# Kernel tuning notes

Hardware: AMD Instinct MI355X
Metric: run time of the kernel (lower is better)

## Reference

```python
import jax, jax.numpy as jnp
import numpy as np

N_NODES = 10000
N_EDGES = 128000


def _edge_conv(x, row, col, edge_attr, w1, b1, w2, b2):
    # gather endpoints, concat edge features, 2-layer MLP per edge
    m = jnp.concatenate([x[row], x[col], edge_attr], axis=1)  # [E, 2*in+edge]
    m = jax.nn.relu(m @ w1 + b1) @ w2 + b2                    # [E, out]
    # scatter-mean onto source nodes (flow='target_to_source' -> aggregate on row)
    n = x.shape[0]
    s = jax.ops.segment_sum(m, row, num_segments=n)
    cnt = jax.ops.segment_sum(jnp.ones((row.shape[0], 1), m.dtype), row, num_segments=n)
    out = s / jnp.maximum(cnt, 1.0)
    return out, m


def setup_inputs() -> dict:
    key = jax.random.key(0)
    ks = jax.random.split(key, 24)
    f = jnp.float32

    def lin(kw, kb, fan_in, fan_out):
        lim = 1.0 / np.sqrt(fan_in)
        w = jax.random.uniform(kw, (fan_in, fan_out), f, -lim, lim)
        b = jax.random.uniform(kb, (fan_out,), f, -lim, lim)
        return w, b

    inp = {}
    inp['x_org'] = jax.random.normal(ks[0], (N_NODES, 256), f)
    inp['x_rot'] = jax.random.normal(ks[1], (N_NODES, 4), f)
    inp['edge_index'] = jax.random.randint(ks[2], (2, N_EDGES), 0, N_NODES, jnp.int64 if jax.config.jax_enable_x64 else jnp.int32)
    inp['edge_attr'] = jax.random.normal(ks[3], (N_EDGES, 640), f)
    inp['edge_rot'] = jax.random.normal(ks[4], (N_EDGES, 4), f)

    # conv1: Linear(2*260+644=1164, 64), Linear(64, 64)
    inp['c1_w1'], inp['c1_b1'] = lin(ks[5], ks[6], 1164, 64)
    inp['c1_w2'], inp['c1_b2'] = lin(ks[7], ks[8], 64, 64)
    # conv2: Linear(2*64+704=832, 64), Linear(64, 64)
    inp['c2_w1'], inp['c2_b1'] = lin(ks[9], ks[10], 832, 64)
    inp['c2_w2'], inp['c2_b2'] = lin(ks[11], ks[12], 64, 64)
    # conv3: Linear(2*128+128=384, 64), Linear(64, 64)
    inp['c3_w1'], inp['c3_b1'] = lin(ks[13], ks[14], 384, 64)
    inp['c3_w2'], inp['c3_b2'] = lin(ks[15], ks[16], 64, 64)
    # conv4: Linear(384, 64), Linear(64, 64)
    inp['c4_w1'], inp['c4_b1'] = lin(ks[17], ks[18], 384, 64)
    inp['c4_w2'], inp['c4_b2'] = lin(ks[19], ks[20], 64, 64)
    # lin1: Linear(64, 4)
    inp['lin1_w'], inp['lin1_b'] = lin(ks[21], ks[22], 64, 4)
    # edge_fc: Linear(64, 32) -> ReLU -> Linear(32, 1)
    k23 = jax.random.split(ks[23], 4)
    inp['efc_w1'], inp['efc_b1'] = lin(k23[0], k23[1], 64, 32)
    inp['efc_w2'], inp['efc_b2'] = lin(k23[2], k23[3], 32, 1)
    return inp


def reference(x_org, x_rot, edge_index, edge_attr, edge_rot,
              c1_w1, c1_b1, c1_w2, c1_b2,
              c2_w1, c2_b1, c2_w2, c2_b2,
              c3_w1, c3_b1, c3_w2, c3_b2,
              c4_w1, c4_b1, c4_w2, c4_b2,
              lin1_w, lin1_b, efc_w1, efc_b1, efc_w2, efc_b2):
    node_feat = jnp.concatenate([x_org, x_rot], axis=1)
    edge_feat = jnp.concatenate([edge_attr, edge_rot], axis=1)
    row, col = edge_index[0], edge_index[1]
    E = edge_index.shape[1]

    x1, edge_x1 = _edge_conv(node_feat, row, col, edge_feat, c1_w1, c1_b1, c1_w2, c1_b2)
    edge_x1 = jax.nn.relu(edge_x1)

    x2, edge_x2 = _edge_conv(x1, row, col, jnp.concatenate([edge_attr, edge_x1], axis=1),
                             c2_w1, c2_b1, c2_w2, c2_b2)
    x2 = jax.nn.relu(x2)
    edge_x2 = jax.nn.relu(edge_x2)

    x3, edge_x3 = _edge_conv(jnp.concatenate([x2, x1], axis=1), row, col,
                             jnp.concatenate([edge_x2, edge_x1], axis=1),
                             c3_w1, c3_b1, c3_w2, c3_b2)
    x3 = jax.nn.relu(x3)
    edge_x3 = jax.nn.relu(edge_x3)

    x4, edge_x4 = _edge_conv(jnp.concatenate([x3, x2], axis=1), row, col,
                             jnp.concatenate([edge_x3, edge_x2], axis=1),
                             c4_w1, c4_b1, c4_w2, c4_b2)
    x4 = jax.nn.relu(x4)

    x = x4 @ lin1_w + lin1_b  # [N, 4]
    h = edge_x4[: E // 2] + edge_x4[E // 2:]
    pred_edge_res = jax.nn.relu(h @ efc_w1 + efc_b1) @ efc_w2 + efc_b2  # [E/2, 1]

    # F.normalize(x, p=2, dim=1)
    x = x / jnp.maximum(jnp.linalg.norm(x, axis=1, keepdims=True), 1e-12)
    return x, pred_edge_res
```

## Files before the change

### kernel.cpp

```cpp
#include <hip/hip_runtime.h>
#include <stdint.h>


#define N_NODES 10000
#define N_EDGES 128000
#define E_HALF  64000
#define NBLK    1000

typedef unsigned short u16;

using bf16x8 = __attribute__((ext_vector_type(8))) short;
using f32x4  = __attribute__((ext_vector_type(4))) float;

#define MFMA16(A, B, C) C = __builtin_amdgcn_mfma_f32_16x16x32_bf16(A, B, C, 0, 0, 0)

__device__ __align__(256) float g_acc[N_NODES * 64];
__device__ __align__(256) float g_deg[N_NODES];
__device__ __align__(256) float g_P[N_NODES * 128];
__device__ __align__(256) float g_x1[N_NODES * 64];
__device__ __align__(256) float g_x2[N_NODES * 64];
__device__ __align__(256) float g_x3[N_NODES * 64];
__device__ __align__(256) u16  g_fragA[(size_t)NBLK * 16384];
__device__ __align__(256) u16  g_fragB[(size_t)NBLK * 16384];
__device__ __align__(256) float g_Q2 [(size_t)N_EDGES * 64];
__device__ __align__(256) float g_ex4[(size_t)N_EDGES * 64];
__device__ __align__(256) u16  g_wpA_hi[2 * 4096];
__device__ __align__(256) u16  g_wpA_lo[2 * 4096];
__device__ __align__(256) u16  g_wp2_hi[4096];
__device__ __align__(256) u16  g_wp2_lo[4096];
__device__ __align__(256) u16  g_wnp_hi[4 * 8192];
__device__ __align__(256) u16  g_wnp_lo[4 * 8192];
__device__ __align__(256) u16  g_wpC_hi[10 * 8192];
__device__ __align__(256) u16  g_wpC_lo[10 * 8192];
__device__ __align__(256) int g_row[N_EDGES];
__device__ __align__(256) int g_col[N_EDGES];
__device__ int g_mode;
__device__ int g_is64;

__device__ __forceinline__ float b2f(u16 u) {
    return __uint_as_float(((unsigned int)u) << 16);
}
__device__ __forceinline__ u16 f2b(float f) {
    unsigned int u = __float_as_uint(f);
    u += 0x7FFFu + ((u >> 16) & 1u);
    return (u16)(u >> 16);
}
__device__ __forceinline__ float ldf(const u16* p)   { return b2f(*p); }
__device__ __forceinline__ float ldf(const float* p) { return *p; }
__device__ __forceinline__ void  stf(u16* p, float v)   { *p = f2b(v); }
__device__ __forceinline__ void  stf(float* p, float v) { *p = v; }

__device__ __forceinline__ float4 load4(const float* p) { return *(const float4*)p; }
__device__ __forceinline__ float4 load4(const u16* p) {
    ushort4 v = *(const ushort4*)p;
    return make_float4(b2f(v.x), b2f(v.y), b2f(v.z), b2f(v.w));
}

template<int KTB>
__device__ __forceinline__ int swz(int b) {
    return b ^ ((b >> 4) & 3) ^ (((b >> KTB) & 1) << 2);
}

__device__ __forceinline__ void split_pack(float4 v, uint2& hi, uint2& lo) {
    unsigned int ux = __float_as_uint(v.x), uy = __float_as_uint(v.y);
    unsigned int uz = __float_as_uint(v.z), uw = __float_as_uint(v.w);
    unsigned int hx = ux & 0xFFFF0000u, hy = uy & 0xFFFF0000u;
    unsigned int hz = uz & 0xFFFF0000u, hw = uw & 0xFFFF0000u;
    hi.x = (hx >> 16) | hy;
    hi.y = (hz >> 16) | hw;
    u16 lx = f2b(v.x - __uint_as_float(hx));
    u16 ly = f2b(v.y - __uint_as_float(hy));
    u16 lz = f2b(v.z - __uint_as_float(hz));
    u16 lw = f2b(v.w - __uint_as_float(hw));
    lo.x = (unsigned int)lx | ((unsigned int)ly << 16);
    lo.y = (unsigned int)lz | ((unsigned int)lw << 16);
}

__global__ void detect_kernel(const void* x_org_v, const int* __restrict__ eidx) {
    const u16* w = (const u16*)x_org_v;
    const int t = threadIdx.x;
    int ok = 0;
    for (int i = t; i < 128; i += 64) {
        u16 v = w[i];
        int ex = (v >> 7) & 0xFF;
        ok += ((ex >= 0x68 && ex <= 0x88) || ((v & 0x7FFFu) == 0)) ? 1 : 0;
    }
    #pragma unroll
    for (int off = 32; off >= 1; off >>= 1) ok += __shfl_xor(ok, off);
    bool allz = true;
    for (int i = t; i < 2048; i += 64) allz = allz && (eidx[2 * i + 1] == 0);
    unsigned long long m = __ballot(allz);
    if (t == 0) {
        g_mode = (ok >= 110) ? 0 : 1;
        g_is64 = (m == ~0ull) ? 1 : 0;
    }
}

__global__ void cvt_idx(const int* __restrict__ eidx) {
    const int e = blockIdx.x * 256 + threadIdx.x;
    if (g_is64) {
        g_row[e] = eidx[2 * e];
        g_col[e] = eidx[2 * (e + N_EDGES)];
    } else {
        g_row[e] = eidx[e];
        g_col[e] = eidx[e + N_EDGES];
    }
}

__global__ void zero_all() {
    const int i = blockIdx.x * 256 + threadIdx.x;
    g_acc[i] = 0.f;
    if (i < N_NODES) g_deg[i] = 0.f;
}

__global__ void deg_kernel() {
    const int e = blockIdx.x * 256 + threadIdx.x;
    if (e < N_EDGES) atomicAdd(&g_deg[g_row[e]], 1.0f);
}

template<typename TW>
__device__ void pack_w_body(const TW* w1a, const TW* w2, const TW* w1b,
                            int we, int ns, int hioff, int nsn, int nsc) {
    const int idx = blockIdx.x * 256 + threadIdx.x;
    const int t1 = ns * 4096;
    const int t2 = t1 + 4096;
    const int t3 = t2 + nsn * 8192;
    if (idx < t1) {
        const int s = idx >> 12;
        const int rem = idx & 4095;
        const int kt = rem >> 11, ct = (rem >> 9) & 3, l = (rem >> 3) & 63, r = rem & 7;
        const int k = s * 64 + kt * 32 + 4 * (l >> 4) + (r & 3) + 16 * (r >> 2);
        const float v = ldf(w1a + (size_t)(we + k) * 64 + ct * 16 + (l & 15));
        const u16 hh = f2b(v);
        g_wpA_hi[idx] = hh;
        g_wpA_lo[idx] = f2b(v - b2f(hh));
    } else if (idx < t2) {
        const int rem = idx - t1;
        const int kt = rem >> 11, ct = (rem >> 9) & 3, l = (rem >> 3) & 63, r = rem & 7;
        const int k = kt * 32 + 4 * (l >> 4) + (r & 3) + 16 * (r >> 2);
        const float v = ldf(w2 + (size_t)k * 64 + ct * 16 + (l & 15));
        const u16 hh = f2b(v);
        g_wp2_hi[rem] = hh;
        g_wp2_lo[rem] = f2b(v - b2f(hh));
    } else if (idx < t3) {
        const int rem = idx - t2;
        const int s = rem >> 13;
        const int kt = (rem >> 12) & 1, ct = (rem >> 9) & 7, l = (rem >> 3) & 63, r = rem & 7;
        const int k = s * 64 + kt * 32 + 4 * (l >> 4) + (r & 3) + 16 * (r >> 2);
        const int col = ct * 16 + (l & 15);
        const int row = (col < 64) ? k : (hioff + k);
        const float v = ldf(w1a + (size_t)row * 64 + (col & 63));
        const u16 hh = f2b(v);
        g_wnp_hi[rem] = hh;
        g_wnp_lo[rem] = f2b(v - b2f(hh));
    } else if (idx < t3 + nsc * 8192) {
        const int rem = idx - t3;
        const int s = rem >> 13;
        const int kt = (rem >> 12) & 1, ct = (rem >> 9) & 7, l = (rem >> 3) & 63, r = rem & 7;
        const int k = s * 64 + kt * 32 + 4 * (l >> 4) + (r & 3) + 16 * (r >> 2);
        const int col = ct * 16 + (l & 15);
        float v;
        if (col < 64) v = ldf(w1a + (size_t)(520 + k) * 64 + col);
        else          v = ldf(w1b + (size_t)(128 + k) * 64 + (col - 64));
        const u16 hh = f2b(v);
        g_wpC_hi[rem] = hh;
        g_wpC_lo[rem] = f2b(v - b2f(hh));
    }
}
__global__ void pack_w_k(const void* w1a, const void* w2, const void* w1b,
                         int we, int ns, int hioff, int nsn, int nsc) {
    if (g_mode == 0)
        pack_w_body<u16>((const u16*)w1a, (const u16*)w2, (const u16*)w1b,
                         we, ns, hioff, nsn, nsc);
    else
        pack_w_body<float>((const float*)w1a, (const float*)w2, (const float*)w1b,
                         we, ns, hioff, nsn, nsc);
}

template<typename TA, int NS1, int NS2, bool TAIL>
__device__ void node_mfma_body(u16* smA, float* smrot, float* smwt,
        const TA* A1, const float* A2, const TA* rotsrc, const TA* w1, float* P) {
    constexpr int NS = NS1 + NS2;
    const int t = threadIdx.x;
    const int lane = t & 63, wid = t >> 6;
    const int q = lane >> 4, n = lane & 15;
    const int r0b = blockIdx.x * 64;

    if constexpr (TAIL) {
        if (t < 64) {
            const int rr = min(r0b + t, N_NODES - 1);
            float4 v = load4(rotsrc + (size_t)rr * 4);
            smrot[t * 4 + 0] = v.x; smrot[t * 4 + 1] = v.y;
            smrot[t * 4 + 2] = v.z; smrot[t * 4 + 3] = v.w;
        }
        for (int i = t; i < 512; i += 256) {
            const int j = i >> 7, c = i & 127;
            const int row = (c < 64) ? (256 + j) : (516 + j);
            smwt[i] = ldf(w1 + (size_t)row * 64 + (c & 63));
        }
    }

    f32x4 acc[8];
    #pragma unroll
    for (int ct = 0; ct < 8; ++ct) acc[ct] = (f32x4){0.f, 0.f, 0.f, 0.f};

    const int eb = t >> 4;
    const int cc = t & 15;

    for (int s = 0; s < NS; ++s) {
        #pragma unroll
        for (int p = 0; p < 4; ++p) {
            const int e = p * 16 + eb;
            const int row = min(r0b + e, N_NODES - 1);
            float4 v;
            if constexpr (NS2 > 0)
                v = (s < NS1) ? load4(A1 + (size_t)row * (NS1 * 64) + s * 64 + cc * 4)
                              : load4(A2 + (size_t)row * (NS2 * 64) + (s - NS1) * 64 + cc * 4);
            else
                v = load4(A1 + (size_t)row * (NS1 * 64) + s * 64 + cc * 4);
            uint2 hi, lo; split_pack(v, hi, lo);
            const int blk = ((cc >> 3) * 4 + (e >> 4)) * 64 + (cc & 3) * 16 + (e & 15);
            const int elem = swz<8>(blk) * 8 + ((cc >> 2) & 1) * 4;
            *(uint2*)&smA[elem]        = hi;
            *(uint2*)&smA[elem + 4096] = lo;
        }
        __syncthreads();
        const u16* wph = g_wnp_hi + s * 8192;
        const u16* wpl = g_wnp_lo + s * 8192;
        #pragma unroll
        for (int kt = 0; kt < 2; ++kt) {
            const int ad = swz<8>((kt * 4 + wid) * 64 + lane) * 8;
            bf16x8 ah = *(const bf16x8*)&smA[ad];
            bf16x8 al = *(const bf16x8*)&smA[ad + 4096];
            #pragma unroll
            for (int ct = 0; ct < 8; ++ct) {
                bf16x8 bh = *(const bf16x8*)&wph[(kt * 8 + ct) * 512 + lane * 8];
                bf16x8 bl = *(const bf16x8*)&wpl[(kt * 8 + ct) * 512 + lane * 8];
                MFMA16(ah, bh, acc[ct]);
                MFMA16(al, bh, acc[ct]);
                MFMA16(ah, bl, acc[ct]);
            }
        }
        __syncthreads();
    }

    #pragma unroll
    for (int ct = 0; ct < 8; ++ct) {
        #pragma unroll
        for (int i = 0; i < 4; ++i) {
            const int rl = wid * 16 + 4 * q + i;
            const int row = r0b + rl;
            const int col = ct * 16 + n;
            float v = acc[ct][i];
            if constexpr (TAIL)
                v += smrot[rl * 4 + 0] * smwt[0 * 128 + col]
                   + smrot[rl * 4 + 1] * smwt[1 * 128 + col]
                   + smrot[rl * 4 + 2] * smwt[2 * 128 + col]
                   + smrot[rl * 4 + 3] * smwt[3 * 128 + col];
            if (row < N_NODES) P[(size_t)row * 128 + col] = v;
        }
    }
}

template<int NS1, bool TAIL>
__global__ void __launch_bounds__(256) node_mfma_in(
        const void* A1, const void* rotsrc, const void* w1, float* __restrict__ P) {
    __shared__ u16 smA[8192];
    __shared__ float smrot[256], smwt[512];
    if (g_mode == 0)
        node_mfma_body<u16, NS1, 0, TAIL>(smA, smrot, smwt, (const u16*)A1,
            nullptr, (const u16*)rotsrc, (const u16*)w1, P);
    else
        node_mfma_body<float, NS1, 0, TAIL>(smA, smrot, smwt, (const float*)A1,
            nullptr, (const float*)rotsrc, (const float*)w1, P);
}

template<int NS1, int NS2>
__global__ void __launch_bounds__(256) node_mfma_ws(
        const float* A1, const float* A2, float* __restrict__ P) {
    __shared__ u16 smA[8192];
    __shared__ float smrot[256], smwt[512];
    node_mfma_body<float, NS1, NS2, false>(smA, smrot, smwt, A1, A2,
        (const float*)nullptr, (const float*)nullptr, P);
}

__device__ __forceinline__ void frag_store_o(u16* smA, int wid, int lane,
        const f32x4 (&oacc)[2][4], u16* Fdst, int blkid) {
    const int q = lane >> 4, n = lane & 15;
    #pragma unroll
    for (int rt = 0; rt < 2; ++rt)
        #pragma unroll
        for (int ct = 0; ct < 4; ++ct)
            #pragma unroll
            for (int i = 0; i < 4; ++i) {
                float v = fmaxf(oacc[rt][ct][i], 0.f);
                unsigned int hb = __float_as_uint(v) & 0xFFFF0000u;
                const u16 hh = (u16)(hb >> 16);
                const u16 hl = f2b(v - __uint_as_float(hb));
                const int off = wid * 4096
                              + (((ct >> 1) * 2 + rt) * 64 + (n >> 2) * 16 + 4 * q + i) * 8
                              + (ct & 1) * 4 + (n & 3);
                smA[off]        = hh;
                smA[off + 2048] = hl;
            }
    #pragma unroll
    for (int kt = 0; kt < 2; ++kt)
        #pragma unroll
        for (int rtl = 0; rtl < 2; ++rtl) {
            const int src = wid * 4096 + ((kt * 2 + rtl) * 64 + lane) * 8;
            bf16x8 h8 = *(const bf16x8*)&smA[src];
            bf16x8 l8 = *(const bf16x8*)&smA[src + 2048];
            const size_t gb = (size_t)blkid * 16384
                            + (size_t)(kt * 8 + wid * 2 + rtl) * 512 + lane * 8;
            *(bf16x8*)&Fdst[gb]        = h8;
            *(bf16x8*)&Fdst[gb + 8192] = l8;
        }
}

template<typename TA, typename TW>
__device__ void edge_c1_body(u16* smA, int* srow, int* scol,
        float* b1s, float* b2s, float* rot, float* wtl,
        const TA* efa, const TA* rotsrc,
        const TW* w1, const TW* b1v, const TW* b2v) {
    const int t = threadIdx.x;
    const int lane = t & 63, wid = t >> 6;
    const int q = lane >> 4, n = lane & 15;
    const int e0 = blockIdx.x * 128;

    if (t < 128) srow[t] = g_row[e0 + t];
    else         scol[t - 128] = g_col[e0 + t - 128];
    if (t >= 128 && t < 192) b1s[t - 128] = ldf(b1v + (t - 128));
    if (t >= 192)            b2s[t - 192] = ldf(b2v + (t - 192));
    if (t < 128) {
        float4 r4 = load4(rotsrc + (size_t)(e0 + t) * 4);
        rot[t * 4 + 0] = r4.x; rot[t * 4 + 1] = r4.y;
        rot[t * 4 + 2] = r4.z; rot[t * 4 + 3] = r4.w;
    }
    wtl[t] = ldf(w1 + (size_t)(1160 + (t >> 6)) * 64 + (t & 63));

    f32x4 acc[2][8];
    #pragma unroll
    for (int a_ = 0; a_ < 2; ++a_)
        #pragma unroll
        for (int b_ = 0; b_ < 8; ++b_)
            acc[a_][b_] = (f32x4){0.f, 0.f, 0.f, 0.f};

    const int eb = t >> 4;
    const int cc = t & 15;

    for (int s = 0; s < 10; ++s) {
        #pragma unroll
        for (int p = 0; p < 8; ++p) {
            const int e = p * 16 + eb;
            float4 v = load4(efa + (size_t)(e0 + e) * 640 + s * 64 + cc * 4);
            uint2 hi, lo; split_pack(v, hi, lo);
            const int blk = ((cc >> 3) * 8 + (e >> 4)) * 64 + (cc & 3) * 16 + (e & 15);
            const int elem = swz<9>(blk) * 8 + ((cc >> 2) & 1) * 4;
            *(uint2*)&smA[elem]        = hi;
            *(uint2*)&smA[elem + 8192] = lo;
        }
        __syncthreads();
        const u16* wph = g_wpC_hi + s * 8192;
        const u16* wpl = g_wpC_lo + s * 8192;
        #pragma unroll
        for (int kt = 0; kt < 2; ++kt) {
            const int b0 = (kt * 8 + wid * 2 + 0) * 64 + lane;
            const int b1i = (kt * 8 + wid * 2 + 1) * 64 + lane;
            const int r0 = swz<9>(b0) * 8;
            const int r1 = swz<9>(b1i) * 8;
            bf16x8 ah0 = *(const bf16x8*)&smA[r0];
            bf16x8 ah1 = *(const bf16x8*)&smA[r1];
            bf16x8 al0 = *(const bf16x8*)&smA[r0 + 8192];
            bf16x8 al1 = *(const bf16x8*)&smA[r1 + 8192];
            #pragma unroll
            for (int ct = 0; ct < 8; ++ct) {
                bf16x8 bh = *(const bf16x8*)&wph[(kt * 8 + ct) * 512 + lane * 8];
                bf16x8 bl = *(const bf16x8*)&wpl[(kt * 8 + ct) * 512 + lane * 8];
                MFMA16(ah0, bh, acc[0][ct]);
                MFMA16(ah1, bh, acc[1][ct]);
                MFMA16(al0, bh, acc[0][ct]);
                MFMA16(al1, bh, acc[1][ct]);
                MFMA16(ah0, bl, acc[0][ct]);
                MFMA16(ah1, bl, acc[1][ct]);
            }
        }
        __syncthreads();
    }

    #pragma unroll
    for (int rt = 0; rt < 2; ++rt)
        #pragma unroll
        for (int c2 = 0; c2 < 4; ++c2)
            #pragma unroll
            for (int i = 0; i < 4; ++i) {
                const int rl = wid * 32 + rt * 16 + 4 * q + i;
                g_Q2[(size_t)(e0 + rl) * 64 + c2 * 16 + n] = acc[rt][4 + c2][i];
            }

    #pragma unroll
    for (int rt = 0; rt < 2; ++rt)
        #pragma unroll
        for (int ct = 0; ct < 4; ++ct)
            #pragma unroll
            for (int i = 0; i < 4; ++i) {
                const int rl = wid * 32 + rt * 16 + 4 * q + i;
                const int col = ct * 16 + n;
                float v = acc[rt][ct][i] + b1s[col]
                        + g_P[(size_t)srow[rl] * 128 + col]
                        + g_P[(size_t)scol[rl] * 128 + 64 + col]
                        + rot[rl * 4 + 0] * wtl[0 * 64 + col]
                        + rot[rl * 4 + 1] * wtl[1 * 64 + col]
                        + rot[rl * 4 + 2] * wtl[2 * 64 + col]
                        + rot[rl * 4 + 3] * wtl[3 * 64 + col];
                v = fmaxf(v, 0.f);
                unsigned int hb = __float_as_uint(v) & 0xFFFF0000u;
                const u16 hh = (u16)(hb >> 16);
                const u16 hl = f2b(v - __uint_as_float(hb));
                const int off = wid * 4096
                              + (((ct >> 1) * 2 + rt) * 64 + (n >> 2) * 16 + 4 * q + i) * 8
                              + (ct & 1) * 4 + (n & 3);
                smA[off]        = hh;
                smA[off + 2048] = hl;
            }

    f32x4 oacc[2][4];
    #pragma unroll
    for (int rt = 0; rt < 2; ++rt)
        #pragma unroll
        for (int ct = 0; ct < 4; ++ct) {
            const float bb = b2s[ct * 16 + n];
            oacc[rt][ct] = (f32x4){bb, bb, bb, bb};
        }
    #pragma unroll
    for (int kt = 0; kt < 2; ++kt) {
        const int r0 = wid * 4096 + ((kt * 2 + 0) * 64 + lane) * 8;
        const int r1 = wid * 4096 + ((kt * 2 + 1) * 64 + lane) * 8;
        bf16x8 ah0 = *(const bf16x8*)&smA[r0];
        bf16x8 ah1 = *(const bf16x8*)&smA[r1];
        bf16x8 al0 = *(const bf16x8*)&smA[r0 + 2048];
        bf16x8 al1 = *(const bf16x8*)&smA[r1 + 2048];
        #pragma unroll
        for (int ct = 0; ct < 4; ++ct) {
            bf16x8 bh = *(const bf16x8*)&g_wp2_hi[(kt * 4 + ct) * 512 + lane * 8];
            bf16x8 bl = *(const bf16x8*)&g_wp2_lo[(kt * 4 + ct) * 512 + lane * 8];
            MFMA16(ah0, bh, oacc[0][ct]);
            MFMA16(ah1, bh, oacc[1][ct]);
            MFMA16(al0, bh, oacc[0][ct]);
            MFMA16(al1, bh, oacc[1][ct]);
            MFMA16(ah0, bl, oacc[0][ct]);
            MFMA16(ah1, bl, oacc[1][ct]);
        }
    }

    #pragma unroll
    for (int rt = 0; rt < 2; ++rt)
        #pragma unroll
        for (int ct = 0; ct < 4; ++ct)
            #pragma unroll
            for (int i = 0; i < 4; ++i) {
                const int rl = wid * 32 + rt * 16 + 4 * q + i;
                atomicAdd(&g_acc[(size_t)srow[rl] * 64 + ct * 16 + n], oacc[rt][ct][i]);
            }
    frag_store_o(smA, wid, lane, oacc, g_fragA, blockIdx.x);
}

__global__ void __launch_bounds__(256, 3) edge_c1(
        const void* efa, const void* rotsrc,
        const void* w1, const void* b1, const void* b2) {
    __shared__ u16 smA[16384];
    __shared__ int srow[128], scol[128];
    __shared__ float b1s[64], b2s[64], rot[512], wtl[256];
    if (g_mode == 0)
        edge_c1_body<u16, u16>(smA, srow, scol, b1s, b2s, rot, wtl,
            (const u16*)efa, (const u16*)rotsrc,
            (const u16*)w1, (const u16*)b1, (const u16*)b2);
    else
        edge_c1_body<float, float>(smA, srow, scol, b1s, b2s, rot, wtl,
            (const float*)efa, (const float*)rotsrc,
            (const float*)w1, (const float*)b1, (const float*)b2);
}

template<typename TW, int NSF, bool HASQ2, bool FRAG_OUT>
__device__ void edge_lite_body(u16* smA, int* srow, int* scol,
        float* b1s, float* b2s,
        const u16* f0, const u16* f1,
        const TW* b1v, const TW* b2v, u16* Ffrag, float* fout) {
    const int t = threadIdx.x;
    const int lane = t & 63, wid = t >> 6;
    const int q = lane >> 4, n = lane & 15;
    const int e0 = blockIdx.x * 128;
    const size_t blkb = (size_t)blockIdx.x * 16384;

    if (t < 128) srow[t] = g_row[e0 + t];
    else         scol[t - 128] = g_col[e0 + t - 128];
    if (t >= 128 && t < 192) b1s[t - 128] = ldf(b1v + (t - 128));
    if (t >= 192)            b2s[t - 192] = ldf(b2v + (t - 192));
    __syncthreads();

    f32x4 acc[2][4];
    #pragma unroll
    for (int a_ = 0; a_ < 2; ++a_)
        #pragma unroll
        for (int b_ = 0; b_ < 4; ++b_)
            acc[a_][b_] = (f32x4){0.f, 0.f, 0.f, 0.f};

    #pragma unroll
    for (int s = 0; s < NSF; ++s) {
        const u16* fs = (s == 0) ? f0 : f1;
        const u16* wph = g_wpA_hi + s * 4096;
        const u16* wpl = g_wpA_lo + s * 4096;
        #pragma unroll
        for (int kt = 0; kt < 2; ++kt) {
            const size_t ba0 = blkb + (size_t)(kt * 8 + wid * 2 + 0) * 512 + lane * 8;
            const size_t ba1 = blkb + (size_t)(kt * 8 + wid * 2 + 1) * 512 + lane * 8;
            bf16x8 ah0 = *(const bf16x8*)&fs[ba0];
            bf16x8 al0 = *(const bf16x8*)&fs[ba0 + 8192];
            bf16x8 ah1 = *(const bf16x8*)&fs[ba1];
            bf16x8 al1 = *(const bf16x8*)&fs[ba1 + 8192];
            #pragma unroll
            for (int ct = 0; ct < 4; ++ct) {
                bf16x8 bh = *(const bf16x8*)&wph[(kt * 4 + ct) * 512 + lane * 8];
                bf16x8 bl = *(const bf16x8*)&wpl[(kt * 4 + ct) * 512 + lane * 8];
                MFMA16(ah0, bh, acc[0][ct]);
                MFMA16(ah1, bh, acc[1][ct]);
                MFMA16(al0, bh, acc[0][ct]);
                MFMA16(al1, bh, acc[1][ct]);
                MFMA16(ah0, bl, acc[0][ct]);
                MFMA16(ah1, bl, acc[1][ct]);
            }
        }
    }

    #pragma unroll
    for (int rt = 0; rt < 2; ++rt)
        #pragma unroll
        for (int ct = 0; ct < 4; ++ct)
            #pragma unroll
            for (int i = 0; i < 4; ++i) {
                const int rl = wid * 32 + rt * 16 + 4 * q + i;
                const int col = ct * 16 + n;
                float v = acc[rt][ct][i] + b1s[col]
                        + g_P[(size_t)srow[rl] * 128 + col]
                        + g_P[(size_t)scol[rl] * 128 + 64 + col];
                if constexpr (HASQ2)
                    v += g_Q2[(size_t)(e0 + rl) * 64 + col];
                v = fmaxf(v, 0.f);
                unsigned int hb = __float_as_uint(v) & 0xFFFF0000u;
                const u16 hh = (u16)(hb >> 16);
                const u16 hl = f2b(v - __uint_as_float(hb));
                const int off = wid * 4096
                              + (((ct >> 1) * 2 + rt) * 64 + (n >> 2) * 16 + 4 * q + i) * 8
                              + (ct & 1) * 4 + (n & 3);
                smA[off]        = hh;
                smA[off + 2048] = hl;
            }

    f32x4 oacc[2][4];
    #pragma unroll
    for (int rt = 0; rt < 2; ++rt)
        #pragma unroll
        for (int ct = 0; ct < 4; ++ct) {
            const float bb = b2s[ct * 16 + n];
            oacc[rt][ct] = (f32x4){bb, bb, bb, bb};
        }
    #pragma unroll
    for (int kt = 0; kt < 2; ++kt) {
        const int r0 = wid * 4096 + ((kt * 2 + 0) * 64 + lane) * 8;
        const int r1 = wid * 4096 + ((kt * 2 + 1) * 64 + lane) * 8;
        bf16x8 ah0 = *(const bf16x8*)&smA[r0];
        bf16x8 ah1 = *(const bf16x8*)&smA[r1];
        bf16x8 al0 = *(const bf16x8*)&smA[r0 + 2048];
        bf16x8 al1 = *(const bf16x8*)&smA[r1 + 2048];
        #pragma unroll
        for (int ct = 0; ct < 4; ++ct) {
            bf16x8 bh = *(const bf16x8*)&g_wp2_hi[(kt * 4 + ct) * 512 + lane * 8];
            bf16x8 bl = *(const bf16x8*)&g_wp2_lo[(kt * 4 + ct) * 512 + lane * 8];
            MFMA16(ah0, bh, oacc[0][ct]);
            MFMA16(ah1, bh, oacc[1][ct]);
            MFMA16(al0, bh, oacc[0][ct]);
            MFMA16(al1, bh, oacc[1][ct]);
            MFMA16(ah0, bl, oacc[0][ct]);
            MFMA16(ah1, bl, oacc[1][ct]);
        }
    }

    #pragma unroll
    for (int rt = 0; rt < 2; ++rt)
        #pragma unroll
        for (int ct = 0; ct < 4; ++ct)
            #pragma unroll
            for (int i = 0; i < 4; ++i) {
                const int rl = wid * 32 + rt * 16 + 4 * q + i;
                const int col = ct * 16 + n;
                const float v = oacc[rt][ct][i];
                atomicAdd(&g_acc[(size_t)srow[rl] * 64 + col], v);
                if constexpr (!FRAG_OUT)
                    fout[(size_t)(e0 + rl) * 64 + col] = v;
            }
    if constexpr (FRAG_OUT)
        frag_store_o(smA, wid, lane, oacc, Ffrag, blockIdx.x);
}

template<int NSF, bool HASQ2, bool FRAG_OUT>
__global__ void __launch_bounds__(256, 4) edge_lite(
        const u16* f0, const u16* f1, const void* b1, const void* b2,
        u16* Ffrag, float* fout) {
    __shared__ u16 smA[16384];
    __shared__ int srow[128], scol[128];
    __shared__ float b1s[64], b2s[64];
    if (g_mode == 0)
        edge_lite_body<u16, NSF, HASQ2, FRAG_OUT>(smA, srow, scol, b1s, b2s,
            f0, f1, (const u16*)b1, (const u16*)b2, Ffrag, fout);
    else
        edge_lite_body<float, NSF, HASQ2, FRAG_OUT>(smA, srow, scol, b1s, b2s,
            f0, f1, (const float*)b1, (const float*)b2, Ffrag, fout);
}

template<bool RELU>
__global__ void finalize_k(float* __restrict__ dst) {
    const int idx = blockIdx.x * 256 + threadIdx.x;
    float v = g_acc[idx] / fmaxf(g_deg[idx >> 6], 1.0f);
    g_acc[idx] = 0.f;
    if (RELU) v = fmaxf(v, 0.f);
    dst[idx] = v;
}

template<typename T>
__device__ void final_node_body(const T* w, const T* b, T* out) {
    const int t = threadIdx.x;
    const int lane = t & 63;
    const int n = blockIdx.x * 4 + (t >> 6);
    float inv = 1.0f / fmaxf(g_deg[n], 1.0f);
    float x4 = fmaxf(g_acc[(size_t)n * 64 + lane] * inv, 0.0f);
    float r[4];
    #pragma unroll
    for (int j = 0; j < 4; ++j) {
        float v = x4 * ldf(w + lane * 4 + j);
        #pragma unroll
        for (int off = 32; off >= 1; off >>= 1) v += __shfl_xor(v, off);
        r[j] = v + ldf(b + j);
    }
    float nrm = sqrtf(r[0]*r[0] + r[1]*r[1] + r[2]*r[2] + r[3]*r[3]);
    float dn = fmaxf(nrm, 1e-12f);
    if (lane < 4) stf(out + n * 4 + lane, r[lane] / dn);
}
__global__ void final_node(const void* w, const void* b, void* out) {
    if (g_mode == 0) final_node_body<u16>((const u16*)w, (const u16*)b, (u16*)out);
    else             final_node_body<float>((const float*)w, (const float*)b, (float*)out);
}

template<typename T>
__device__ void edge_head_body(const float* ex4, const T* w1, const T* b1,
                               const T* w2, const T* b2, T* out) {
    __shared__ float lw1[2048];
    __shared__ float lw2[32];
    const int t = threadIdx.x;
    for (int i = t; i < 2048; i += 256) lw1[i] = ldf(w1 + i);
    if (t < 32) lw2[t] = ldf(w2 + t);
    __syncthreads();
    const int e = blockIdx.x * 256 + t;
    float a[32];
    #pragma unroll
    for (int j = 0; j < 32; ++j) a[j] = ldf(b1 + j);
    const float* p0 = ex4 + (size_t)e * 64;
    const float* p1 = ex4 + (size_t)(e + E_HALF) * 64;
    for (int c = 0; c < 64; ++c) {
        float h = p0[c] + p1[c];
        #pragma unroll
        for (int j = 0; j < 32; ++j) a[j] += h * lw1[c * 32 + j];
    }
    float s = ldf(b2);
    #pragma unroll
    for (int j = 0; j < 32; ++j) s += fmaxf(a[j], 0.f) * lw2[j];
    stf(out + e, s);
}
__global__ void __launch_bounds__(256) edge_head(const float* ex4,
        const void* w1, const void* b1, const void* w2, const void* b2,
        void* out) {
    if (g_mode == 0)
        edge_head_body<u16>(ex4, (const u16*)w1, (const u16*)b1,
                            (const u16*)w2, (const u16*)b2, (u16*)out + 40000);
    else
        edge_head_body<float>(ex4, (const float*)w1, (const float*)b1,
                              (const float*)w2, (const float*)b2, (float*)out + 40000);
}

__global__ void sentinel_fill(unsigned int* out, int n_words) {
    int i = blockIdx.x * 256 + threadIdx.x;
    if (i < n_words) out[i] = 0x44794479u;
}

static void* sym_addr(const void* symbol) {
    void* p = nullptr;
    (void)hipGetSymbolAddress(&p, symbol);
    return p;
}

extern "C" void kernel_launch(void* const* d_in, const int* in_sizes, int n_in,
                              void* d_out, int out_size, void* d_ws, size_t ws_size,
                              hipStream_t stream) {
    (void)d_ws; (void)ws_size;
    bool ok = (n_in == 27) && (out_size == 104000)
           && (in_sizes[0] == 2560000) && (in_sizes[2] == 256000)
           && (in_sizes[3] == 81920000) && (in_sizes[5] == 74496)
           && (in_sizes[21] == 256) && (in_sizes[25] == 32);
    if (!ok) {
        sentinel_fill<<<204, 256, 0, stream>>>((unsigned int*)d_out, 52000);
        return;
    }
    const void* x_org     = d_in[0];
    const void* x_rot     = d_in[1];
    const int*  eidx      = (const int*)d_in[2];
    const void* edge_attr = d_in[3];
    const void* edge_rot  = d_in[4];

    float* P   = (float*)sym_addr(HIP_SYMBOL(g_P));
    float* x1  = (float*)sym_addr(HIP_SYMBOL(g_x1));
    float* x2  = (float*)sym_addr(HIP_SYMBOL(g_x2));
    float* x3  = (float*)sym_addr(HIP_SYMBOL(g_x3));
    u16*   fA  = (u16*)sym_addr(HIP_SYMBOL(g_fragA));
    u16*   fB  = (u16*)sym_addr(HIP_SYMBOL(g_fragB));
    float* ex4 = (float*)sym_addr(HIP_SYMBOL(g_ex4));

    detect_kernel<<<1, 64, 0, stream>>>(x_org, eidx);
    cvt_idx<<<500, 256, 0, stream>>>(eidx);
    zero_all<<<2500, 256, 0, stream>>>();
    deg_kernel<<<500, 256, 0, stream>>>();

    pack_w_k<<<464, 256, 0, stream>>>(d_in[5], d_in[7], d_in[9], 0, 0, 260, 4, 10);
    node_mfma_in<4, true><<<157, 256, 0, stream>>>(x_org, x_rot, d_in[5], P);
    edge_c1<<<NBLK, 256, 0, stream>>>(edge_attr, edge_rot, d_in[5], d_in[6], d_in[8]);
    finalize_k<false><<<2500, 256, 0, stream>>>(x1);

    pack_w_k<<<64, 256, 0, stream>>>(d_in[9], d_in[11], d_in[9], 768, 1, 64, 1, 0);
    node_mfma_ws<1, 0><<<157, 256, 0, stream>>>(x1, nullptr, P);
    edge_lite<1, true, true><<<NBLK, 256, 0, stream>>>(
        fA, nullptr, d_in[10], d_in[12], fB, nullptr);
    finalize_k<true><<<2500, 256, 0, stream>>>(x2);

    pack_w_k<<<112, 256, 0, stream>>>(d_in[13], d_in[15], d_in[13], 256, 2, 128, 2, 0);
    node_mfma_ws<1, 1><<<157, 256, 0, stream>>>(x2, x1, P);
    edge_lite<2, false, true><<<NBLK, 256, 0, stream>>>(
        fB, fA, d_in[14], d_in[16], fA, nullptr);
    finalize_k<true><<<2500, 256, 0, stream>>>(x3);

    pack_w_k<<<112, 256, 0, stream>>>(d_in[17], d_in[19], d_in[17], 256, 2, 128, 2, 0);
    node_mfma_ws<1, 1><<<157, 256, 0, stream>>>(x3, x2, P);
    edge_lite<2, false, false><<<NBLK, 256, 0, stream>>>(
        fA, fB, d_in[18], d_in[20], nullptr, ex4);

    final_node<<<2500, 256, 0, stream>>>(d_in[21], d_in[22], d_out);
    edge_head<<<250, 256, 0, stream>>>(ex4, d_in[23], d_in[24], d_in[25], d_in[26],
                                       d_out);
}
```

Before: 943.1 us.

## Load MFMA A-fragments directly from global into registers, drop LDS staging

```diff
diff --git a/kernel.cpp b/kernel.cpp
--- a/kernel.cpp
+++ b/kernel.cpp
@@ -56,11 +56,6 @@
     return make_float4(b2f(v.x), b2f(v.y), b2f(v.z), b2f(v.w));
 }
 
-template<int KTB>
-__device__ __forceinline__ int swz(int b) {
-    return b ^ ((b >> 4) & 3) ^ (((b >> KTB) & 1) << 2);
-}
-
 __device__ __forceinline__ void split_pack(float4 v, uint2& hi, uint2& lo) {
     unsigned int ux = __float_as_uint(v.x), uy = __float_as_uint(v.y);
     unsigned int uz = __float_as_uint(v.z), uw = __float_as_uint(v.w);
@@ -74,6 +69,17 @@
     u16 lw = f2b(v.w - __uint_as_float(hw));
     lo.x = (unsigned int)lx | ((unsigned int)ly << 16);
     lo.y = (unsigned int)lz | ((unsigned int)lw << 16);
+}
+
+__device__ __forceinline__ void mk_frag(float4 v0, float4 v1,
+                                        bf16x8& fh, bf16x8& fl) {
+    uint2 h0, l0, h1, l1;
+    split_pack(v0, h0, l0);
+    split_pack(v1, h1, l1);
+    union { unsigned int w[4]; bf16x8 v; } H, L;
+    H.w[0] = h0.x; H.w[1] = h0.y; H.w[2] = h1.x; H.w[3] = h1.y;
+    L.w[0] = l0.x; L.w[1] = l0.y; L.w[2] = l1.x; L.w[3] = l1.y;
+    fh = H.v; fl = L.v;
 }
 
 __global__ void detect_kernel(const void* x_org_v, const int* __restrict__ eidx) {
@@ -178,7 +184,7 @@
 }
 
 template<typename TA, int NS1, int NS2, bool TAIL>
-__device__ void node_mfma_body(u16* smA, float* smrot, float* smwt,
+__device__ void node_mfma_body(float* smrot, float* smwt,
         const TA* A1, const float* A2, const TA* rotsrc, const TA* w1, float* P) {
     constexpr int NS = NS1 + NS2;
     const int t = threadIdx.x;
@@ -198,40 +204,32 @@
             const int row = (c < 64) ? (256 + j) : (516 + j);
             smwt[i] = ldf(w1 + (size_t)row * 64 + (c & 63));
         }
-    }
+        __syncthreads();
+    }
+
+    const int arow = min(r0b + wid * 16 + n, N_NODES - 1);
 
     f32x4 acc[8];
     #pragma unroll
     for (int ct = 0; ct < 8; ++ct) acc[ct] = (f32x4){0.f, 0.f, 0.f, 0.f};
 
-    const int eb = t >> 4;
-    const int cc = t & 15;
-
+    #pragma unroll
     for (int s = 0; s < NS; ++s) {
         #pragma unroll
-        for (int p = 0; p < 4; ++p) {
-            const int e = p * 16 + eb;
-            const int row = min(r0b + e, N_NODES - 1);
-            float4 v;
-            if constexpr (NS2 > 0)
-                v = (s < NS1) ? load4(A1 + (size_t)row * (NS1 * 64) + s * 64 + cc * 4)
-                              : load4(A2 + (size_t)row * (NS2 * 64) + (s - NS1) * 64 + cc * 4);
-            else
-                v = load4(A1 + (size_t)row * (NS1 * 64) + s * 64 + cc * 4);
-            uint2 hi, lo; split_pack(v, hi, lo);
-            const int blk = ((cc >> 3) * 4 + (e >> 4)) * 64 + (cc & 3) * 16 + (e & 15);
-            const int elem = swz<8>(blk) * 8 + ((cc >> 2) & 1) * 4;
-            *(uint2*)&smA[elem]        = hi;
-            *(uint2*)&smA[elem + 4096] = lo;
-        }
-        __syncthreads();
-        const u16* wph = g_wnp_hi + s * 8192;
-        const u16* wpl = g_wnp_lo + s * 8192;
-        #pragma unroll
         for (int kt = 0; kt < 2; ++kt) {
-            const int ad = swz<8>((kt * 4 + wid) * 64 + lane) * 8;
-            bf16x8 ah = *(const bf16x8*)&smA[ad];
-            bf16x8 al = *(const bf16x8*)&smA[ad + 4096];
+            float4 v0, v1;
+            if (s < NS1) {
+                const TA* p = A1 + (size_t)arow * (NS1 * 64) + s * 64 + kt * 32 + q * 4;
+                v0 = load4(p); v1 = load4(p + 16);
+            } else {
+                const float* p = A2 + (size_t)arow * (NS2 * 64) + (s - NS1) * 64
+                               + kt * 32 + q * 4;
+                v0 = load4(p); v1 = load4(p + 16);
+            }
+            bf16x8 ah, al;
+            mk_frag(v0, v1, ah, al);
+            const u16* wph = g_wnp_hi + s * 8192;
+            const u16* wpl = g_wnp_lo + s * 8192;
             #pragma unroll
             for (int ct = 0; ct < 8; ++ct) {
                 bf16x8 bh = *(const bf16x8*)&wph[(kt * 8 + ct) * 512 + lane * 8];
@@ -241,7 +239,6 @@
                 MFMA16(ah, bl, acc[ct]);
             }
         }
-        __syncthreads();
     }
 
     #pragma unroll
@@ -265,22 +262,20 @@
 template<int NS1, bool TAIL>
 __global__ void __launch_bounds__(256) node_mfma_in(
         const void* A1, const void* rotsrc, const void* w1, float* __restrict__ P) {
-    __shared__ u16 smA[8192];
     __shared__ float smrot[256], smwt[512];
     if (g_mode == 0)
-        node_mfma_body<u16, NS1, 0, TAIL>(smA, smrot, smwt, (const u16*)A1,
+        node_mfma_body<u16, NS1, 0, TAIL>(smrot, smwt, (const u16*)A1,
             nullptr, (const u16*)rotsrc, (const u16*)w1, P);
     else
-        node_mfma_body<float, NS1, 0, TAIL>(smA, smrot, smwt, (const float*)A1,
+        node_mfma_body<float, NS1, 0, TAIL>(smrot, smwt, (const float*)A1,
             nullptr, (const float*)rotsrc, (const float*)w1, P);
 }
 
 template<int NS1, int NS2>
 __global__ void __launch_bounds__(256) node_mfma_ws(
         const float* A1, const float* A2, float* __restrict__ P) {
-    __shared__ u16 smA[8192];
     __shared__ float smrot[256], smwt[512];
-    node_mfma_body<float, NS1, NS2, false>(smA, smrot, smwt, A1, A2,
+    node_mfma_body<float, NS1, NS2, false>(smrot, smwt, A1, A2,
         (const float*)nullptr, (const float*)nullptr, P);
 }
 
@@ -337,6 +332,7 @@
         rot[t * 4 + 2] = r4.z; rot[t * 4 + 3] = r4.w;
     }
     wtl[t] = ldf(w1 + (size_t)(1160 + (t >> 6)) * 64 + (t & 63));
+    __syncthreads();
 
     f32x4 acc[2][8];
     #pragma unroll
@@ -345,33 +341,27 @@
         for (int b_ = 0; b_ < 8; ++b_)
             acc[a_][b_] = (f32x4){0.f, 0.f, 0.f, 0.f};
 
-    const int eb = t >> 4;
-    const int cc = t & 15;
-
-    for (int s = 0; s < 10; ++s) {
-        #pragma unroll
-        for (int p = 0; p < 8; ++p) {
-            const int e = p * 16 + eb;
-            float4 v = load4(efa + (size_t)(e0 + e) * 640 + s * 64 + cc * 4);
-            uint2 hi, lo; split_pack(v, hi, lo);
-            const int blk = ((cc >> 3) * 8 + (e >> 4)) * 64 + (cc & 3) * 16 + (e & 15);
-            const int elem = swz<9>(blk) * 8 + ((cc >> 2) & 1) * 4;
-            *(uint2*)&smA[elem]        = hi;
-            *(uint2*)&smA[elem + 8192] = lo;
-        }
-        __syncthreads();
+    const TA* arow0 = efa + (size_t)(e0 + wid * 32 + n) * 640;
+    const TA* arow1 = efa + (size_t)(e0 + wid * 32 + 16 + n) * 640;
+
+    auto issue = [&](float4 (&buf)[2][2][2], int s) {
+        const int cb = s * 64 + q * 4;
+        #pragma unroll
+        for (int kt = 0; kt < 2; ++kt) {
+            buf[0][kt][0] = load4(arow0 + cb + kt * 32);
+            buf[0][kt][1] = load4(arow0 + cb + kt * 32 + 16);
+            buf[1][kt][0] = load4(arow1 + cb + kt * 32);
+            buf[1][kt][1] = load4(arow1 + cb + kt * 32 + 16);
+        }
+    };
+    auto step = [&](float4 (&buf)[2][2][2], int s) {
         const u16* wph = g_wpC_hi + s * 8192;
         const u16* wpl = g_wpC_lo + s * 8192;
         #pragma unroll
         for (int kt = 0; kt < 2; ++kt) {
-            const int b0 = (kt * 8 + wid * 2 + 0) * 64 + lane;
-            const int b1i = (kt * 8 + wid * 2 + 1) * 64 + lane;
-            const int r0 = swz<9>(b0) * 8;
-            const int r1 = swz<9>(b1i) * 8;
-            bf16x8 ah0 = *(const bf16x8*)&smA[r0];
-            bf16x8 ah1 = *(const bf16x8*)&smA[r1];
-            bf16x8 al0 = *(const bf16x8*)&smA[r0 + 8192];
-            bf16x8 al1 = *(const bf16x8*)&smA[r1 + 8192];
+            bf16x8 ah0, al0, ah1, al1;
+            mk_frag(buf[0][kt][0], buf[0][kt][1], ah0, al0);
+            mk_frag(buf[1][kt][0], buf[1][kt][1], ah1, al1);
             #pragma unroll
             for (int ct = 0; ct < 8; ++ct) {
                 bf16x8 bh = *(const bf16x8*)&wph[(kt * 8 + ct) * 512 + lane * 8];
@@ -384,7 +374,15 @@
                 MFMA16(ah1, bl, acc[1][ct]);
             }
         }
-        __syncthreads();
+    };
+
+    float4 bufA[2][2][2], bufB[2][2][2];
+    issue(bufA, 0);
+    for (int s = 0; s < 10; s += 2) {
+        issue(bufB, s + 1);
+        step(bufA, s);
+        if (s + 2 < 10) issue(bufA, s + 2);
+        step(bufB, s + 1);
     }
 
     #pragma unroll
```

Result: faster. 896.3 us (-5.0%).
